# Optimization experiments

Hardware: AMD Instinct MI355X
Metric: run time of the kernel (lower is better)

The kernel has to match this reference:

```python
import jax, jax.numpy as jnp
import numpy as np

N, T, C, H, W = 16, 8, 256, 14, 14
IC = 64          # inter_channels
SCALE = 32       # nearest-upsample factor (scale_s); scale_t = 1


def setup_inputs() -> dict:
    key = jax.random.key(0)
    kx, kq1, kq2, kv1, kl, ki = jax.random.split(key, 6)
    cin = C + 1
    x = jax.random.normal(kx, (N, T, C, H, W), dtype=jnp.float32)
    lam = jax.random.uniform(kl, (), dtype=jnp.float32)
    index = jax.random.randint(ki, (N,), 0, N)
    # nn.Linear default init: U(-1/sqrt(fan_in), 1/sqrt(fan_in))
    bound = 1.0 / np.sqrt(cin)
    Wq = jax.random.uniform(kq1, (IC, cin), minval=-bound, maxval=bound, dtype=jnp.float32)
    bq = jax.random.uniform(kq2, (IC,), minval=-bound, maxval=bound, dtype=jnp.float32)
    Wv = jax.random.uniform(kv1, (1, cin), minval=-bound, maxval=bound, dtype=jnp.float32)
    Wv = Wv.at[0, C].set(4.0)   # value.weight.data[0, in_channel] = 4
    bv = jnp.zeros((1,), dtype=jnp.float32)  # value.bias.data[:] = 0
    return {"x": x, "lam": lam, "index": index, "Wq": Wq, "bq": bq, "Wv": Wv, "bv": bv}


def reference(x, lam, index, Wq, bq, Wv, bv):
    n, t, c, h, w = x.shape
    ic = Wq.shape[0]
    nt, hw = n * t, h * w
    x_lam = x.reshape(nt, c, h, w)
    x_lam_ = x[index].reshape(nt, c, h, w)           # batch-shuffled partner
    lam_block = jnp.broadcast_to(lam - 0.5, (nt, 1, h, w)).astype(x.dtype)
    x_lam = jnp.concatenate([x_lam, lam_block], axis=1)     # [nt, c+1, h, w]
    x_lam_ = jnp.concatenate([x_lam_, -lam_block], axis=1)
    # linear over channel dim (equivalent to the transpose(1,3)/Linear/transpose dance)
    q = jnp.einsum('nchw,dc->ndhw', x_lam, Wq) + bq[None, :, None, None]
    k = jnp.einsum('nchw,dc->ndhw', x_lam_, Wq) + bq[None, :, None, None]
    v = jnp.einsum('nchw,dc->ndhw', x_lam_, Wv) + bv[None, :, None, None]
    q_x = q.reshape(nt, ic, hw).transpose(0, 2, 1)   # [nt, hw, ic]
    k_x = k.reshape(nt, ic, hw)                      # [nt, ic, hw]
    v_ = v.reshape(nt, 1, hw).transpose(0, 2, 1)     # [nt, hw, 1]
    scores = jnp.einsum('nqd,ndk->nqk', q_x, k_x) / jnp.sqrt(jnp.float32(ic))
    attn = jax.nn.softmax(scores, axis=-1)           # [nt, hw, hw]
    mask_lam_ = jnp.matmul(attn.astype(jnp.float32), v_.astype(jnp.float32))
    mask_lam_ = mask_lam_.reshape(nt, 1, h, w)       # scale_t == 1 so expand is a no-op
    # F.interpolate(mode='nearest', scale_factor=SCALE)
    mask_lam_ = jnp.repeat(jnp.repeat(mask_lam_, SCALE, axis=2), SCALE, axis=3)
    mask_lam_ = jax.nn.sigmoid(mask_lam_)
    mask = jnp.concatenate([1.0 - mask_lam_, mask_lam_], axis=1)  # [nt, 2, h*S, w*S]
    v_out = v_.reshape(n, t, h, w)                    # (n, t*scale_t, h, w)
    return mask, v_out
```

## Files before the change

### kernel.cpp

```cpp
#include <hip/hip_runtime.h>
#include <hip/hip_bf16.h>
#include <stdint.h>

#define HWsz 196
#define NTs  128
#define MASK_ELEMS 51380224
#define VOUT_OFF   MASK_ELEMS

#define EQ_OFF_F 3221504
#define EK_OFF_F 4024704
#define V_OFF    4827904

typedef __attribute__((ext_vector_type(8))) short short8;
typedef __attribute__((ext_vector_type(4))) float f32x4;

__device__ __forceinline__ bool is_bf16_mode(const void* wv) {
  return ((const uint16_t*)wv)[256] == (uint16_t)0x4080;
}

__device__ __forceinline__ float ldf(const void* p, int i, bool bf) {
  if (bf) {
    uint32_t u = (uint32_t)((const uint16_t*)p)[i] << 16;
    return __builtin_bit_cast(float, u);
  }
  return ((const float*)p)[i];
}

__device__ __forceinline__ uint16_t f2bf(float f) {
  __hip_bfloat16 h = __float2bfloat16(f);
  return __builtin_bit_cast(uint16_t, h);
}

__device__ __forceinline__ float bf2f(uint16_t u) {
  uint32_t v = (uint32_t)u << 16;
  return __builtin_bit_cast(float, v);
}

#define AST 116

template<int NMT, int NCOLS, int J0>
__device__ __forceinline__ void k1_body(uint16_t* Abuf, uint16_t* Bbuf,
    const void* xraw, const int* index, const void* Wqraw, const void* bqraw,
    const void* Wvraw, const void* bvraw, const void* lamraw,
    float* ws, void* dout, int b) {
  int s = b & 127, isK = (b >> 7) & 1;
  int t = s & 7;
  int src = isK ? index[s >> 3] * 8 + t : s;
  bool bf = is_bf16_mode(Wvraw);
  int tid = threadIdx.x;
  int lane = tid & 63, w = tid >> 6;
  int ln = lane & 15, quad = lane >> 4;
  int d = w * 16 + ln;
  size_t xbase = (size_t)src * 256 * 196;

  f32x4 acc[NMT];
#pragma unroll
  for (int mt = 0; mt < NMT; mt++) acc[mt] = (f32x4){0.f, 0.f, 0.f, 0.f};
  float vacc = 0.f;
  int cS1 = tid >> 2, jjS1 = tid & 3;
  int c2S = tid >> 3, jtS = tid & 7;

#pragma unroll 1
  for (int chunk = 0; chunk < 4; chunk++) {
    short8 bw0, bw1;
    {
      int cb = d * 257 + chunk * 64 + quad * 8;
#pragma unroll
      for (int e = 0; e < 8; e++) {
        bw0[e] = (short)f2bf(ldf(Wqraw, cb + e, bf));
        bw1[e] = (short)f2bf(ldf(Wqraw, cb + 32 + e, bf));
      }
    }
    __syncthreads();
    if (bf) {
      const uint16_t* xp = (const uint16_t*)xraw + xbase +
                           (size_t)(chunk * 64 + cS1) * 196 + J0;
      for (int jj = jjS1; jj * 4 < NCOLS; jj += 4)
        *(uint2*)(Abuf + cS1 * AST + jj * 4) = *(const uint2*)(xp + jj * 4);
    } else {
      const float* xp = (const float*)xraw + xbase +
                        (size_t)(chunk * 64 + cS1) * 196 + J0;
      for (int jj = jjS1; jj * 4 < NCOLS; jj += 4) {
        float4 v4 = *(const float4*)(xp + jj * 4);
        uint2 pk;
        pk.x = (uint32_t)f2bf(v4.x) | ((uint32_t)f2bf(v4.y) << 16);
        pk.y = (uint32_t)f2bf(v4.z) | ((uint32_t)f2bf(v4.w) << 16);
        *(uint2*)(Abuf + cS1 * AST + jj * 4) = pk;
      }
    }
    __syncthreads();
    for (int j = jtS; j < NCOLS; j += 8) {
      uint32_t lo = Abuf[(2 * c2S) * AST + j];
      uint32_t hi = Abuf[(2 * c2S + 1) * AST + j];
      int gp = (c2S >> 2) ^ (j & 7);
      ((uint32_t*)Bbuf)[j * 32 + gp * 4 + (c2S & 3)] = lo | (hi << 16);
    }
    __syncthreads();
#pragma unroll
    for (int kc2 = 0; kc2 < 2; kc2++) {
      short8 bfrag = kc2 ? bw1 : bw0;
#pragma unroll
      for (int mt = 0; mt < NMT; mt++) {
        int j = mt * 16 + ln;
        short8 afrag = *(const short8*)(Bbuf + j * 64 +
                                        (((kc2 * 4 + quad) ^ (j & 7)) << 3));
        acc[mt] = __builtin_amdgcn_mfma_f32_16x16x32_bf16(afrag, bfrag, acc[mt], 0, 0, 0);
      }
    }
    if (isK && tid < NCOLS) {
#pragma unroll 8
      for (int c = 0; c < 64; c++)
        vacc = fmaf(bf2f(Abuf[c * AST + tid]), ldf(Wvraw, chunk * 64 + c, bf), vacc);
    }
  }

  float lamv = ldf(lamraw, 0, bf) - 0.5f;
  float lamch = isK ? -lamv : lamv;
  float addend = ldf(Wqraw, d * 257 + 256, bf) * lamch + ldf(bqraw, d, bf);
  uint16_t* E = (uint16_t*)(ws + (isK ? EK_OFF_F : EQ_OFF_F));
#pragma unroll
  for (int mt = 0; mt < NMT; mt++) {
#pragma unroll
    for (int r = 0; r < 4; r++) {
      int j = J0 + mt * 16 + quad * 4 + r;
      if (j < HWsz) E[((size_t)s * HWsz + j) * 64 + d] = f2bf(acc[mt][r] + addend);
    }
  }

  if (isK && tid < NCOLS) {
    int j = J0 + tid;
    float vvv = vacc + ldf(Wvraw, 256, bf) * lamch + ldf(bvraw, 0, bf);
    ws[V_OFF + s * HWsz + j] = vvv;
    if (bf) ((uint16_t*)dout)[VOUT_OFF + s * HWsz + j] = f2bf(vvv);
    else    ((float*)dout)[VOUT_OFF + s * HWsz + j] = vvv;
  }
}

__global__ __launch_bounds__(256) void k1_qk(const void* xraw, const int* index,
    const void* Wqraw, const void* bqraw, const void* Wvraw, const void* bvraw,
    const void* lamraw, float* ws, void* dout) {
  __shared__ __align__(16) uint16_t Abuf[64 * AST];
  __shared__ __align__(16) uint16_t Bbuf[112 * 64];
  int b = blockIdx.x;
  if (b < 256)
    k1_body<7, 112, 0>(Abuf, Bbuf, xraw, index, Wqraw, bqraw, Wvraw, bvraw, lamraw, ws, dout, b);
  else
    k1_body<6, 84, 112>(Abuf, Bbuf, xraw, index, Wqraw, bqraw, Wvraw, bvraw, lamraw, ws, dout, b & 255);
}

__global__ __launch_bounds__(256) void k2_attn_mask(float* ws, void* dout, const void* Wvraw) {
  __shared__ float sig[64];
  bool bf = is_bf16_mode(Wvraw);
  int s = blockIdx.x >> 2, blk = blockIdx.x & 3;
  int tid = threadIdx.x;
  int lane = tid & 63, w = tid >> 6;
  int mt = blk * 4 + w;
  int ln = lane & 15, quad = lane >> 4;

  if (mt < 13) {
    const uint16_t* Eq = (const uint16_t*)(ws + EQ_OFF_F);
    const uint16_t* Ek = (const uint16_t*)(ws + EK_OFF_F);
    const uint16_t* qrow = Eq + ((size_t)s * 196 + mt * 16 + ln) * 64 + quad * 8;
    short8 aq0 = *(const short8*)(qrow);
    short8 aq1 = *(const short8*)(qrow + 32);

    float vcol[13];
    f32x4 acc[13];
#pragma unroll
    for (int nt = 0; nt < 13; nt++) {
      int col = nt * 16 + ln;
      vcol[nt] = (col < 196) ? ws[V_OFF + s * 196 + col] : 0.f;
      const uint16_t* krow = Ek + ((size_t)s * 196 + col) * 64 + quad * 8;
      short8 b0 = *(const short8*)(krow);
      short8 b1 = *(const short8*)(krow + 32);
      f32x4 a = (f32x4){0.f, 0.f, 0.f, 0.f};
      a = __builtin_amdgcn_mfma_f32_16x16x32_bf16(aq0, b0, a, 0, 0, 0);
      a = __builtin_amdgcn_mfma_f32_16x16x32_bf16(aq1, b1, a, 0, 0, 0);
      acc[nt] = a;
    }

    float mx[4] = {-1e30f, -1e30f, -1e30f, -1e30f};
#pragma unroll
    for (int nt = 0; nt < 13; nt++) {
      bool valid = (nt * 16 + ln) < 196;
#pragma unroll
      for (int r = 0; r < 4; r++) {
        float sv = valid ? acc[nt][r] * 0.125f : -1e30f;
        acc[nt][r] = sv;
        mx[r] = fmaxf(mx[r], sv);
      }
    }
#pragma unroll
    for (int m = 1; m < 16; m <<= 1)
#pragma unroll
      for (int r = 0; r < 4; r++) mx[r] = fmaxf(mx[r], __shfl_xor(mx[r], m));

    float l[4] = {0.f, 0.f, 0.f, 0.f}, av[4] = {0.f, 0.f, 0.f, 0.f};
#pragma unroll
    for (int nt = 0; nt < 13; nt++)
#pragma unroll
      for (int r = 0; r < 4; r++) {
        float p = __expf(acc[nt][r] - mx[r]);
        l[r] += p;
        av[r] += p * vcol[nt];
      }
#pragma unroll
    for (int m = 1; m < 16; m <<= 1)
#pragma unroll
      for (int r = 0; r < 4; r++) {
        l[r] += __shfl_xor(l[r], m);
        av[r] += __shfl_xor(av[r], m);
      }

    if (ln == 0) {
#pragma unroll
      for (int r = 0; r < 4; r++) {
        int j = mt * 16 + quad * 4 + r;
        if (j < 196) {
          float mval = av[r] / l[r];
          sig[j & 63] = 1.f / (1.f + __expf(-mval));
        }
      }
    }
  }
  __syncthreads();

  int j0 = blk * 64;
  int nrows = (blk == 3) ? 4 : 64;
  int base2 = s * 2;
  if (!bf) {
    float4* o4 = (float4*)dout;
    int total = nrows << 9;
    for (int i = tid; i < total; i += 256) {
      int x4 = i & 7, dy = (i >> 3) & 31, ch = (i >> 8) & 1, jl = i >> 9;
      int j = j0 + jl;
      int yhw = j / 14, xhw = j - yhw * 14;
      float v = sig[jl];
      if (!ch) v = 1.f - v;
      size_t off4 = (size_t)(base2 + ch) * 50176 + (yhw * 32 + dy) * 112 + (xhw << 3) + x4;
      o4[off4] = make_float4(v, v, v, v);
    }
  } else {
    uint4* o = (uint4*)dout;
    int total = nrows << 8;
    for (int i = tid; i < total; i += 256) {
      int x4 = i & 3, dy = (i >> 2) & 31, ch = (i >> 7) & 1, jl = i >> 8;
      int j = j0 + jl;
      int yhw = j / 14, xhw = j - yhw * 14;
      float v = sig[jl];
      if (!ch) v = 1.f - v;
      uint32_t ub = (uint32_t)f2bf(v), pk = ub | (ub << 16);
      size_t off = (size_t)(base2 + ch) * 25088 + (yhw * 32 + dy) * 56 + (xhw << 2) + x4;
      o[off] = (uint4){pk, pk, pk, pk};
    }
  }
}

extern "C" void kernel_launch(void* const* d_in, const int* in_sizes, int n_in,
                              void* d_out, int out_size, void* d_ws, size_t ws_size,
                              hipStream_t stream) {
  const void* x   = d_in[0];
  const void* lam = d_in[1];
  const int* idx  = (const int*)d_in[2];
  const void* Wq  = d_in[3];
  const void* bq  = d_in[4];
  const void* Wv  = d_in[5];
  const void* bv  = d_in[6];
  float* ws = (float*)d_ws;

  k1_qk<<<512, 256, 0, stream>>>(x, idx, Wq, bq, Wv, bv, lam, ws, d_out);
  k2_attn_mask<<<512, 256, 0, stream>>>(ws, d_out, Wv);
}
```

Before: 265.9 us.

## Use LDS transpose reads for MFMA operands and restructure v projection and mask stores

Stages x tiles in LDS in a layout that ds_read_b64_tr_b16 can transpose directly into MFMA A fragments. This drops the explicit shared-memory transpose pass and one barrier per chunk. The value projection now reads x straight from global memory with four independent accumulators instead of from the staged LDS tile. The mask writer stores two 16-byte vectors per thread iteration, halving the loop trip count. The risks are the inline asm correctness and the extra global traffic in the v loop.

```diff
diff --git a/kernel.cpp b/kernel.cpp
--- a/kernel.cpp
+++ b/kernel.cpp
@@ -3,7 +3,6 @@
 #include <stdint.h>
 
 #define HWsz 196
-#define NTs  128
 #define MASK_ELEMS 51380224
 #define VOUT_OFF   MASK_ELEMS
 
@@ -12,6 +11,7 @@
 #define V_OFF    4827904
 
 typedef __attribute__((ext_vector_type(8))) short short8;
+typedef __attribute__((ext_vector_type(4))) short short4v;
 typedef __attribute__((ext_vector_type(4))) float f32x4;
 
 __device__ __forceinline__ bool is_bf16_mode(const void* wv) {
@@ -36,16 +36,13 @@
   return __builtin_bit_cast(float, v);
 }
 
-#define AST 116
-
 template<int NMT, int NCOLS, int J0>
-__device__ __forceinline__ void k1_body(uint16_t* Abuf, uint16_t* Bbuf,
+__device__ __forceinline__ void k1_body(uint16_t* Abuf,
     const void* xraw, const int* index, const void* Wqraw, const void* bqraw,
     const void* Wvraw, const void* bvraw, const void* lamraw,
     float* ws, void* dout, int b) {
   int s = b & 127, isK = (b >> 7) & 1;
-  int t = s & 7;
-  int src = isK ? index[s >> 3] * 8 + t : s;
+  int src = isK ? index[s >> 3] * 8 + (s & 7) : s;
   bool bf = is_bf16_mode(Wvraw);
   int tid = threadIdx.x;
   int lane = tid & 63, w = tid >> 6;
@@ -56,9 +53,8 @@
   f32x4 acc[NMT];
 #pragma unroll
   for (int mt = 0; mt < NMT; mt++) acc[mt] = (f32x4){0.f, 0.f, 0.f, 0.f};
-  float vacc = 0.f;
   int cS1 = tid >> 2, jjS1 = tid & 3;
-  int c2S = tid >> 3, jtS = tid & 7;
+  uint32_t abase = (uint32_t)(uintptr_t)Abuf + (uint32_t)(quad * 128);
 
 #pragma unroll 1
   for (int chunk = 0; chunk < 4; chunk++) {
@@ -76,7 +72,8 @@
       const uint16_t* xp = (const uint16_t*)xraw + xbase +
                            (size_t)(chunk * 64 + cS1) * 196 + J0;
       for (int jj = jjS1; jj * 4 < NCOLS; jj += 4)
-        *(uint2*)(Abuf + cS1 * AST + jj * 4) = *(const uint2*)(xp + jj * 4);
+        *(uint2*)(Abuf + (jj >> 2) * 1024 + cS1 * 16 + (jj & 3) * 4) =
+            *(const uint2*)(xp + jj * 4);
     } else {
       const float* xp = (const float*)xraw + xbase +
                         (size_t)(chunk * 64 + cS1) * 196 + J0;
@@ -85,32 +82,29 @@
         uint2 pk;
         pk.x = (uint32_t)f2bf(v4.x) | ((uint32_t)f2bf(v4.y) << 16);
         pk.y = (uint32_t)f2bf(v4.z) | ((uint32_t)f2bf(v4.w) << 16);
-        *(uint2*)(Abuf + cS1 * AST + jj * 4) = pk;
+        *(uint2*)(Abuf + (jj >> 2) * 1024 + cS1 * 16 + (jj & 3) * 4) = pk;
       }
     }
     __syncthreads();
-    for (int j = jtS; j < NCOLS; j += 8) {
-      uint32_t lo = Abuf[(2 * c2S) * AST + j];
-      uint32_t hi = Abuf[(2 * c2S + 1) * AST + j];
-      int gp = (c2S >> 2) ^ (j & 7);
-      ((uint32_t*)Bbuf)[j * 32 + gp * 4 + (c2S & 3)] = lo | (hi << 16);
-    }
-    __syncthreads();
 #pragma unroll
     for (int kc2 = 0; kc2 < 2; kc2++) {
-      short8 bfrag = kc2 ? bw1 : bw0;
+      short4v lo[NMT], hi[NMT];
 #pragma unroll
       for (int mt = 0; mt < NMT; mt++) {
-        int j = mt * 16 + ln;
-        short8 afrag = *(const short8*)(Bbuf + j * 64 +
-                                        (((kc2 * 4 + quad) ^ (j & 7)) << 3));
-        acc[mt] = __builtin_amdgcn_mfma_f32_16x16x32_bf16(afrag, bfrag, acc[mt], 0, 0, 0);
-      }
-    }
-    if (isK && tid < NCOLS) {
-#pragma unroll 8
-      for (int c = 0; c < 64; c++)
-        vacc = fmaf(bf2f(Abuf[c * AST + tid]), ldf(Wvraw, chunk * 64 + c, bf), vacc);
+        asm volatile("ds_read_b64_tr_b16 %0, %2 offset:%3\n\t"
+                     "ds_read_b64_tr_b16 %1, %2 offset:%4"
+                     : "=v"(lo[mt]), "=v"(hi[mt])
+                     : "v"(abase), "i"(mt * 2048 + kc2 * 1024),
+                       "i"(mt * 2048 + kc2 * 1024 + 128));
+      }
+      asm volatile("s_waitcnt lgkmcnt(0)" ::: "memory");
+      __builtin_amdgcn_sched_barrier(0);
+#pragma unroll
+      for (int mt = 0; mt < NMT; mt++) {
+        short8 af = __builtin_shufflevector(lo[mt], hi[mt], 0, 1, 2, 3, 4, 5, 6, 7);
+        acc[mt] = __builtin_amdgcn_mfma_f32_16x16x32_bf16(af, kc2 ? bw1 : bw0,
+                                                          acc[mt], 0, 0, 0);
+      }
     }
   }
 
@@ -129,7 +123,27 @@
 
   if (isK && tid < NCOLS) {
     int j = J0 + tid;
-    float vvv = vacc + ldf(Wvraw, 256, bf) * lamch + ldf(bvraw, 0, bf);
+    float vp0 = 0.f, vp1 = 0.f, vp2 = 0.f, vp3 = 0.f;
+    if (bf) {
+      const uint16_t* xp = (const uint16_t*)xraw + xbase + j;
+#pragma unroll 4
+      for (int c = 0; c < 256; c += 4) {
+        vp0 = fmaf(bf2f(xp[(size_t)(c + 0) * 196]), ldf(Wvraw, c + 0, bf), vp0);
+        vp1 = fmaf(bf2f(xp[(size_t)(c + 1) * 196]), ldf(Wvraw, c + 1, bf), vp1);
+        vp2 = fmaf(bf2f(xp[(size_t)(c + 2) * 196]), ldf(Wvraw, c + 2, bf), vp2);
+        vp3 = fmaf(bf2f(xp[(size_t)(c + 3) * 196]), ldf(Wvraw, c + 3, bf), vp3);
+      }
+    } else {
+      const float* xp = (const float*)xraw + xbase + j;
+#pragma unroll 4
+      for (int c = 0; c < 256; c += 4) {
+        vp0 = fmaf(xp[(size_t)(c + 0) * 196], ldf(Wvraw, c + 0, bf), vp0);
+        vp1 = fmaf(xp[(size_t)(c + 1) * 196], ldf(Wvraw, c + 1, bf), vp1);
+        vp2 = fmaf(xp[(size_t)(c + 2) * 196], ldf(Wvraw, c + 2, bf), vp2);
+        vp3 = fmaf(xp[(size_t)(c + 3) * 196], ldf(Wvraw, c + 3, bf), vp3);
+      }
+    }
+    float vvv = (vp0 + vp1) + (vp2 + vp3) + ldf(Wvraw, 256, bf) * lamch + ldf(bvraw, 0, bf);
     ws[V_OFF + s * HWsz + j] = vvv;
     if (bf) ((uint16_t*)dout)[VOUT_OFF + s * HWsz + j] = f2bf(vvv);
     else    ((float*)dout)[VOUT_OFF + s * HWsz + j] = vvv;
@@ -139,13 +153,12 @@
 __global__ __launch_bounds__(256) void k1_qk(const void* xraw, const int* index,
     const void* Wqraw, const void* bqraw, const void* Wvraw, const void* bvraw,
     const void* lamraw, float* ws, void* dout) {
-  __shared__ __align__(16) uint16_t Abuf[64 * AST];
-  __shared__ __align__(16) uint16_t Bbuf[112 * 64];
+  __shared__ __align__(16) uint16_t Abuf[7 * 1024];
   int b = blockIdx.x;
   if (b < 256)
-    k1_body<7, 112, 0>(Abuf, Bbuf, xraw, index, Wqraw, bqraw, Wvraw, bvraw, lamraw, ws, dout, b);
+    k1_body<7, 112, 0>(Abuf, xraw, index, Wqraw, bqraw, Wvraw, bvraw, lamraw, ws, dout, b);
   else
-    k1_body<6, 84, 112>(Abuf, Bbuf, xraw, index, Wqraw, bqraw, Wvraw, bvraw, lamraw, ws, dout, b & 255);
+    k1_body<6, 84, 112>(Abuf, xraw, index, Wqraw, bqraw, Wvraw, bvraw, lamraw, ws, dout, b & 255);
 }
 
 __global__ __launch_bounds__(256) void k2_attn_mask(float* ws, void* dout, const void* Wvraw) {
@@ -230,28 +243,34 @@
   int base2 = s * 2;
   if (!bf) {
     float4* o4 = (float4*)dout;
-    int total = nrows << 9;
+    int total = nrows << 8;
     for (int i = tid; i < total; i += 256) {
-      int x4 = i & 7, dy = (i >> 3) & 31, ch = (i >> 8) & 1, jl = i >> 9;
+      int x2 = i & 3, dy = (i >> 2) & 31, ch = (i >> 7) & 1, jl = i >> 8;
       int j = j0 + jl;
       int yhw = j / 14, xhw = j - yhw * 14;
       float v = sig[jl];
       if (!ch) v = 1.f - v;
-      size_t off4 = (size_t)(base2 + ch) * 50176 + (yhw * 32 + dy) * 112 + (xhw << 3) + x4;
-      o4[off4] = make_float4(v, v, v, v);
+      size_t off4 = (size_t)(base2 + ch) * 50176 +
+                    (size_t)(yhw * 32 + dy) * 112 + (xhw << 3) + (x2 << 1);
+      float4 f = make_float4(v, v, v, v);
+      o4[off4] = f;
+      o4[off4 + 1] = f;
     }
   } else {
     uint4* o = (uint4*)dout;
-    int total = nrows << 8;
+    int total = nrows << 7;
     for (int i = tid; i < total; i += 256) {
-      int x4 = i & 3, dy = (i >> 2) & 31, ch = (i >> 7) & 1, jl = i >> 8;
+      int x2 = i & 1, dy = (i >> 1) & 31, ch = (i >> 6) & 1, jl = i >> 7;
       int j = j0 + jl;
       int yhw = j / 14, xhw = j - yhw * 14;
       float v = sig[jl];
       if (!ch) v = 1.f - v;
       uint32_t ub = (uint32_t)f2bf(v), pk = ub | (ub << 16);
-      size_t off = (size_t)(base2 + ch) * 25088 + (yhw * 32 + dy) * 56 + (xhw << 2) + x4;
-      o[off] = (uint4){pk, pk, pk, pk};
+      uint4 qv; qv.x = pk; qv.y = pk; qv.z = pk; qv.w = pk;
+      size_t off = (size_t)(base2 + ch) * 25088 +
+                   (size_t)(yhw * 32 + dy) * 56 + (xhw << 2) + (x2 << 1);
+      o[off] = qv;
+      o[off + 1] = qv;
     }
   }
 }
```

Result: no change. 265.7 us (-0.1%).
